# Kernel optimization log

Measured on AMD Instinct MI355X. Metric: run time of the kernel, lower is better.

Reference implementation:

```python
import jax, jax.numpy as jnp
import numpy as np

N = 50000      # nodes
E = 800000     # edges
F = 128        # node_features
DSS = 64       # degree_set_size
H = 128        # latent dim (hardcoded in GraphES)


def gcn_conv(x, W, b, src, dst, n):
    # PyG GCNConv: linear -> symmetric-normalized aggregation with self loops -> bias
    h = x @ W                                            # [N, C_out]
    deg = jnp.zeros((n,), x.dtype).at[dst].add(1.0) + 1.0  # in-degree incl. self loop
    dinv = jax.lax.rsqrt(deg)
    norm = dinv[src] * dinv[dst]                         # [E]
    agg = jnp.zeros_like(h).at[dst].add(h[src] * norm[:, None])
    agg = agg + h * (dinv * dinv)[:, None]               # self-loop term (norm_ii = 1/deg_i)
    return agg + b


def mlp(x, w1, b1, w2, b2):
    return jax.nn.relu(x @ w1 + b1) @ w2 + b2


def _swap(ei, i1, i2, coin):
    e1 = jnp.take(ei, i1, axis=1)
    e2 = jnp.take(ei, i2, axis=1)
    a, b = e1[0], e1[1]
    c, d = e2[0], e2[1]
    ne1 = jnp.where(coin, jnp.stack([a, d]), jnp.stack([a, c]))
    ne2 = jnp.where(coin, jnp.stack([c, b]), jnp.stack([b, d]))
    return ei.at[:, i1].set(ne1).at[:, i2].set(ne2)


def setup_inputs() -> dict:
    key = jax.random.key(0)
    ks = jax.random.split(key, 24)
    s = 0.05

    def rn(k, shape):
        return jax.random.normal(k, shape, jnp.float32) * s

    return {
        "x": jax.random.normal(ks[0], (N, F), jnp.float32),
        "edge_index": jax.random.randint(ks[1], (2, E), 0, N, dtype=jnp.int32),
        "degree_set": jax.random.randint(ks[2], (N,), 0, DSS, dtype=jnp.int32),
        "timesteps": 5,
        # encoder: GCN(F+DSS -> 2H), GCN(2H -> H)
        "enc_w1": rn(ks[3], (F + DSS, 2 * H)), "enc_b1": jnp.zeros((2 * H,), jnp.float32),
        "enc_w2": rn(ks[4], (2 * H, H)),       "enc_b2": jnp.zeros((H,), jnp.float32),
        # decoder: GCN(H+DSS -> 2F), GCN(2F -> F)
        "dec_w1": rn(ks[5], (H + DSS, 2 * F)), "dec_b1": jnp.zeros((2 * F,), jnp.float32),
        "dec_w2": rn(ks[6], (2 * F, F)),       "dec_b2": jnp.zeros((F,), jnp.float32),
        # edge_predictor_1: Linear(128,64)->ReLU->Linear(64,1)
        "ep1_w1": rn(ks[7], (H, 64)),  "ep1_b1": jnp.zeros((64,), jnp.float32),
        "ep1_w2": rn(ks[8], (64, 1)),  "ep1_b2": jnp.zeros((1,), jnp.float32),
        # edge_predictor_2: input is z concat flattened pair features -> 128+256=384
        "ep2_w1": rn(ks[9], (H + 2 * H, 64)), "ep2_b1": jnp.zeros((64,), jnp.float32),
        "ep2_w2": rn(ks[10], (64, 1)),        "ep2_b2": jnp.zeros((1,), jnp.float32),
    }


def reference(x, edge_index, degree_set, timesteps,
              enc_w1, enc_b1, enc_w2, enc_b2,
              dec_w1, dec_b1, dec_w2, dec_b2,
              ep1_w1, ep1_b1, ep1_w2, ep1_b2,
              ep2_w1, ep2_b1, ep2_w2, ep2_b2):
    src, dst = edge_index[0], edge_index[1]
    dh = jax.nn.one_hot(degree_set, DSS, dtype=x.dtype)  # [N, DSS]

    # ---- encoder ----
    h = jax.nn.relu(gcn_conv(jnp.concatenate([x, dh], 1), enc_w1, enc_b1, src, dst, N))
    z = gcn_conv(h, enc_w2, enc_b2, src, dst, N)          # [N, H]

    # ---- forward diffusion: timesteps random edge swaps (deterministic PRNG) ----
    ei = edge_index
    for t in range(timesteps):
        k1, k2 = jax.random.split(jax.random.fold_in(jax.random.key(1), t))
        idx = jax.random.choice(k1, E, (2,), replace=False)
        ei = _swap(ei, idx[0], idx[1], jax.random.bernoulli(k2))

    # ---- reverse process: argmax-driven edge swaps ----
    # edge_predictor_1 scores depend only on z -> identical every step; compute once
    i1 = jnp.argmax(mlp(z, ep1_w1, ep1_b1, ep1_w2, ep1_b2).squeeze(-1))
    for t in range(timesteps):
        e1 = jnp.take(ei, i1, axis=1)                     # [2]
        e1f = z[e1].reshape(-1)                           # [2H]
        cond = jnp.concatenate([z, jnp.broadcast_to(e1f, (N, 2 * H))], 1)
        i2 = jnp.argmax(mlp(cond, ep2_w1, ep2_b1, ep2_w2, ep2_b2).squeeze(-1))
        coin = jax.random.bernoulli(jax.random.fold_in(jax.random.key(2), t))
        ei = _swap(ei, i1, i2, coin)

    # ---- decoder on final edge structure ----
    src2, dst2 = ei[0], ei[1]
    hd = jax.nn.relu(gcn_conv(jnp.concatenate([z, dh], 1), dec_w1, dec_b1, src2, dst2, N))
    out = gcn_conv(hd, dec_w2, dec_b2, src2, dst2, N)     # [N, F]
    return out, ei
```

## Files before the change

kernel.cpp:

```cpp
#include <hip/hip_runtime.h>
#include <cstdint>
#include <cstddef>
#include <vector>
#include <algorithm>

#define NN 50000
#define EE 800000
#define FF 128
#define HH 128
#define TSTEPS 5

typedef __attribute__((ext_vector_type(8))) short bf16x8;
typedef __attribute__((ext_vector_type(4))) float f32x4;

__device__ __forceinline__ float bf2f(unsigned short u)
{
    return __uint_as_float((unsigned)u << 16);
}
__device__ __forceinline__ unsigned short f2bf(float x)
{
    unsigned u = __float_as_uint(x);
    u = (u + 0x7FFFu + ((u >> 16) & 1u));
    return (unsigned short)(u >> 16);
}
__device__ __forceinline__ void splitbf(float v, unsigned short& hi, unsigned short& lo)
{
    hi = f2bf(v);
    lo = f2bf(v - bf2f(hi));
}

__device__ __forceinline__ void gload16(const void* g, void* l)
{
    __builtin_amdgcn_global_load_lds(
        (const __attribute__((address_space(1))) void*)g,
        (__attribute__((address_space(3))) void*)l, 16, 0, 0);
}

__global__ __launch_bounds__(256, 4) void zw1_gemm(
    const float* __restrict__ A, const float* __restrict__ Wp4,
    float* __restrict__ Pout, int n, const float* __restrict__ bias)
{
    __shared__ float As[32][128];
    const int row0 = blockIdx.x * 32;
    const int tid = threadIdx.x;
    for (int idx = tid; idx < 32 * 32; idx += 256) {
        int r = idx >> 5, k4 = idx & 31;
        int gr = row0 + r;
        float4 v = make_float4(0.f, 0.f, 0.f, 0.f);
        if (gr < n) v = ((const float4*)(A + (size_t)gr * 128))[k4];
        *(float4*)&As[r][k4 * 4] = v;
    }
    __syncthreads();
    const int w = tid >> 6, l = tid & 63;
    float acc[8];
#pragma unroll
    for (int r = 0; r < 8; r++) acc[r] = 0.f;

#pragma unroll 2
    for (int k4 = 0; k4 < 32; k4++) {
        float4 wv = ((const float4*)Wp4)[k4 * 64 + l];
#pragma unroll
        for (int r = 0; r < 8; r++) {
            float4 zv = *(const float4*)&As[w * 8 + r][k4 * 4];
            acc[r] = fmaf(zv.x, wv.x, acc[r]);
            acc[r] = fmaf(zv.y, wv.y, acc[r]);
            acc[r] = fmaf(zv.z, wv.z, acc[r]);
            acc[r] = fmaf(zv.w, wv.w, acc[r]);
        }
    }
    float bv = bias[l];
#pragma unroll
    for (int r = 0; r < 8; r++) {
        int gr = row0 + w * 8 + r;
        if (gr < n) Pout[(size_t)gr * 64 + l] = acc[r] + bv;
    }
}

template <int K, int C, int BC, int WR, int WC, bool HAS_BIAS, bool RELU>
__global__ __launch_bounds__(256) void gemm_bf16_tiled(
    const unsigned short* __restrict__ A, const unsigned short* __restrict__ Wp,
    unsigned short* __restrict__ Pout, const float* __restrict__ bias, int n)
{
    constexpr int KC = K / 32;
    constexpr int RT = 128 / (WR * 16);
    constexpr int TT = BC / (WC * 16);
    constexpr int STAGE_USHORTS = 4096 + BC * 32;
    constexpr int OT_USHORTS = 128 * BC;
    constexpr int LDS_USHORTS = (STAGE_USHORTS > OT_USHORTS) ? STAGE_USHORTS : OT_USHORTS;
    __shared__ __align__(16) unsigned short smem[LDS_USHORTS];
    unsigned short* AL = smem;
    unsigned short* WL = smem + 4096;

    const int row0 = blockIdx.x * 128;
    const int col0 = blockIdx.y * BC;
    const int tid = threadIdx.x;
    const int w = tid >> 6, l = tid & 63;
    const int m = l & 15, quad = l >> 4;
    const int wr = w / WC, wc = w % WC;
    const int rowBase = wr * (RT * 16);
    const int colBase = wc * (TT * 16);

    f32x4 acc[RT][TT];
#pragma unroll
    for (int rt = 0; rt < RT; rt++)
#pragma unroll
        for (int tt = 0; tt < TT; tt++) acc[rt][tt] = { 0.f, 0.f, 0.f, 0.f };

    for (int kc = 0; kc < KC; kc++) {
        for (int s = w; s < 8; s += 4) {
            int rg = row0 + s * 16 + (l >> 2);
            if (rg > n - 1) rg = n - 1;
            size_t go = (size_t)rg * K + kc * 32 + (l & 3) * 8;
            gload16(A + go, AL + s * 512);
        }
        for (int s = w; s < BC / 16; s += 4) {
            size_t wo = ((size_t)kc * C + col0) * 32 + s * 512 + l * 8;
            gload16(Wp + wo, WL + s * 512);
        }
        __syncthreads();

        bf16x8 a[RT];
#pragma unroll
        for (int rt = 0; rt < RT; rt++)
            a[rt] = *(const bf16x8*)(AL + (rowBase + rt * 16 + m) * 32 + quad * 8);
#pragma unroll
        for (int tt = 0; tt < TT; tt++) {
            bf16x8 b = *(const bf16x8*)(WL + (colBase + tt * 16 + m) * 32 + quad * 8);
#pragma unroll
            for (int rt = 0; rt < RT; rt++)
                acc[rt][tt] = __builtin_amdgcn_mfma_f32_16x16x32_bf16(a[rt], b, acc[rt][tt], 0, 0, 0);
        }
        __syncthreads();
    }

    unsigned short* Ot = smem;
#pragma unroll
    for (int tt = 0; tt < TT; tt++) {
        int col_in = colBase + tt * 16 + m;
        float bv = HAS_BIAS ? bias[col0 + col_in] : 0.f;
#pragma unroll
        for (int rt = 0; rt < RT; rt++)
#pragma unroll
            for (int r = 0; r < 4; r++) {
                int row_in = rowBase + rt * 16 + quad * 4 + r;
                float v = acc[rt][tt][r] + bv;
                if (RELU) v = fmaxf(v, 0.f);
                Ot[row_in * BC + col_in] = f2bf(v);
            }
    }
    __syncthreads();
    for (int idx = tid; idx < 128 * (BC / 8); idx += 256) {
        int rr = idx / (BC / 8), c8 = idx - rr * (BC / 8);
        int gr = row0 + rr;
        if (gr < n)
            *(bf16x8*)(Pout + (size_t)gr * C + col0 + c8 * 8) =
                *(const bf16x8*)(Ot + rr * BC + c8 * 8);
    }
}

template <int K, int C, int BC, int WR, int WC, bool HAS_BIAS, bool RELU, bool OUT_SPLIT>
__global__ __launch_bounds__(256) void gemm_split_tiled(
    const unsigned short* __restrict__ Ahi, const unsigned short* __restrict__ Alo,
    const unsigned short* __restrict__ Whi, const unsigned short* __restrict__ Wlo,
    void* __restrict__ PoutHi, unsigned short* __restrict__ PoutLo,
    const float* __restrict__ bias, int n)
{
    constexpr int KC = K / 32;
    constexpr int RT = 128 / (WR * 16);
    constexpr int TT = BC / (WC * 16);
    constexpr int LDS_USHORTS = 8192 + BC * 64;
    __shared__ __align__(16) unsigned short smem[LDS_USHORTS];
    unsigned short* AhL = smem;
    unsigned short* AlL = smem + 4096;
    unsigned short* WhL = smem + 8192;
    unsigned short* WlL = smem + 8192 + BC * 32;

    const int row0 = blockIdx.x * 128;
    const int col0 = blockIdx.y * BC;
    const int tid = threadIdx.x;
    const int w = tid >> 6, l = tid & 63;
    const int m = l & 15, quad = l >> 4;
    const int wr = w / WC, wc = w % WC;
    const int rowBase = wr * (RT * 16);
    const int colBase = wc * (TT * 16);

    f32x4 acc[RT][TT];
#pragma unroll
    for (int rt = 0; rt < RT; rt++)
#pragma unroll
        for (int tt = 0; tt < TT; tt++) acc[rt][tt] = { 0.f, 0.f, 0.f, 0.f };

    for (int kc = 0; kc < KC; kc++) {
        for (int s = w; s < 8; s += 4) {
            int rg = row0 + s * 16 + (l >> 2);
            if (rg > n - 1) rg = n - 1;
            size_t go = (size_t)rg * K + kc * 32 + (l & 3) * 8;
            gload16(Ahi + go, AhL + s * 512);
            gload16(Alo + go, AlL + s * 512);
        }
        for (int s = w; s < BC / 16; s += 4) {
            size_t wo = ((size_t)kc * C + col0) * 32 + s * 512 + l * 8;
            gload16(Whi + wo, WhL + s * 512);
            gload16(Wlo + wo, WlL + s * 512);
        }
        __syncthreads();

        bf16x8 ah[RT], al[RT];
#pragma unroll
        for (int rt = 0; rt < RT; rt++) {
            int ro = (rowBase + rt * 16 + m) * 32 + quad * 8;
            ah[rt] = *(const bf16x8*)(AhL + ro);
            al[rt] = *(const bf16x8*)(AlL + ro);
        }
#pragma unroll
        for (int tt = 0; tt < TT; tt++) {
            int co = (colBase + tt * 16 + m) * 32 + quad * 8;
            bf16x8 wh = *(const bf16x8*)(WhL + co);
            bf16x8 wl = *(const bf16x8*)(WlL + co);
#pragma unroll
            for (int rt = 0; rt < RT; rt++) {
                acc[rt][tt] = __builtin_amdgcn_mfma_f32_16x16x32_bf16(al[rt], wh, acc[rt][tt], 0, 0, 0);
                acc[rt][tt] = __builtin_amdgcn_mfma_f32_16x16x32_bf16(ah[rt], wl, acc[rt][tt], 0, 0, 0);
                acc[rt][tt] = __builtin_amdgcn_mfma_f32_16x16x32_bf16(ah[rt], wh, acc[rt][tt], 0, 0, 0);
            }
        }
        __syncthreads();
    }

    if (OUT_SPLIT) {
        unsigned short* Ot = smem;
#pragma unroll
        for (int tt = 0; tt < TT; tt++) {
            int col_in = colBase + tt * 16 + m;
            float bv = HAS_BIAS ? bias[col0 + col_in] : 0.f;
#pragma unroll
            for (int rt = 0; rt < RT; rt++)
#pragma unroll
                for (int r = 0; r < 4; r++) {
                    int row_in = rowBase + rt * 16 + quad * 4 + r;
                    float v = acc[rt][tt][r] + bv;
                    if (RELU) v = fmaxf(v, 0.f);
                    Ot[row_in * BC + col_in] = f2bf(v);
                }
        }
        __syncthreads();
        for (int idx = tid; idx < 128 * (BC / 8); idx += 256) {
            int rr = idx / (BC / 8), c8 = idx - rr * (BC / 8);
            int gr = row0 + rr;
            if (gr < n)
                *(bf16x8*)((unsigned short*)PoutHi + (size_t)gr * C + col0 + c8 * 8) =
                    *(const bf16x8*)(Ot + rr * BC + c8 * 8);
        }
        __syncthreads();
#pragma unroll
        for (int tt = 0; tt < TT; tt++) {
            int col_in = colBase + tt * 16 + m;
            float bv = HAS_BIAS ? bias[col0 + col_in] : 0.f;
#pragma unroll
            for (int rt = 0; rt < RT; rt++)
#pragma unroll
                for (int r = 0; r < 4; r++) {
                    int row_in = rowBase + rt * 16 + quad * 4 + r;
                    float v = acc[rt][tt][r] + bv;
                    if (RELU) v = fmaxf(v, 0.f);
                    unsigned short h = f2bf(v);
                    Ot[row_in * BC + col_in] = f2bf(v - bf2f(h));
                }
        }
        __syncthreads();
        for (int idx = tid; idx < 128 * (BC / 8); idx += 256) {
            int rr = idx / (BC / 8), c8 = idx - rr * (BC / 8);
            int gr = row0 + rr;
            if (gr < n)
                *(bf16x8*)(PoutLo + (size_t)gr * C + col0 + c8 * 8) =
                    *(const bf16x8*)(Ot + rr * BC + c8 * 8);
        }
    } else {
#pragma unroll
        for (int tt = 0; tt < TT; tt++) {
            int col = col0 + colBase + tt * 16 + m;
            float bv = HAS_BIAS ? bias[col] : 0.f;
#pragma unroll
            for (int rt = 0; rt < RT; rt++)
#pragma unroll
                for (int r = 0; r < 4; r++) {
                    int gr = row0 + rowBase + rt * 16 + quad * 4 + r;
                    if (gr >= n) continue;
                    float v = acc[rt][tt][r] + bv;
                    if (RELU) v = fmaxf(v, 0.f);
                    ((float*)PoutHi)[(size_t)gr * C + col] = v;
                }
        }
    }
}

template <int K, int C>
__global__ void pack_w(const float* __restrict__ W, unsigned short* __restrict__ Wp)
{
    int idx = blockIdx.x * 256 + threadIdx.x;
    if (idx >= K * C) return;
    int k = idx / C, nn = idx - k * C;
    Wp[((size_t)(k >> 5) * C + nn) * 32 + (k & 31)] = f2bf(W[idx]);
}

template <int K, int C>
__global__ void pack_w_split(const float* __restrict__ W,
                             unsigned short* __restrict__ Wphi,
                             unsigned short* __restrict__ Wplo)
{
    int idx = blockIdx.x * 256 + threadIdx.x;
    if (idx >= K * C) return;
    int k = idx / C, nn = idx - k * C;
    unsigned short hi, lo;
    splitbf(W[idx], hi, lo);
    size_t o = ((size_t)(k >> 5) * C + nn) * 32 + (k & 31);
    Wphi[o] = hi;
    Wplo[o] = lo;
}

template <int K, int C>
__global__ void pack_w4(const float* __restrict__ W, float* __restrict__ Wp4)
{
    int idx = blockIdx.x * 256 + threadIdx.x;
    if (idx >= K * C) return;
    int k = idx / C, c = idx - k * C;
    Wp4[(((size_t)(k >> 2) * C) + c) * 4 + (k & 3)] = W[idx];
}

__global__ void count_deg(const int* __restrict__ dst, int* __restrict__ cnt, int e)
{
    int i = blockIdx.x * blockDim.x + threadIdx.x;
    if (i < e) {
        unsigned d = (unsigned)dst[i];
        if (d < (unsigned)NN) atomicAdd(&cnt[d], 1);
    }
}

__global__ void scan_block(const int* __restrict__ cnt, int* __restrict__ excl,
                           int* __restrict__ bsum, float* __restrict__ dinv, int n)
{
    __shared__ int s[256];
    int i = blockIdx.x * 256 + threadIdx.x;
    int v = (i < n) ? cnt[i] : 0;
    if (i < n) dinv[i] = 1.0f / sqrtf((float)v + 1.0f);
    s[threadIdx.x] = v;
    __syncthreads();
    for (int off = 1; off < 256; off <<= 1) {
        int t = (threadIdx.x >= off) ? s[threadIdx.x - off] : 0;
        __syncthreads();
        s[threadIdx.x] += t;
        __syncthreads();
    }
    if (i < n) excl[i] = s[threadIdx.x] - v;
    if (threadIdx.x == 255) bsum[blockIdx.x] = s[255];
}
__global__ void scan_add_fill(int* __restrict__ rowptr, const int* __restrict__ bsum,
                              int* __restrict__ fill, int n, int e)
{
    int pre = 0;
    for (int b = 0; b < (int)blockIdx.x; b++) pre += bsum[b];
    int i = blockIdx.x * 256 + threadIdx.x;
    if (i < n) { rowptr[i] += pre; fill[i] = 0; }
    if (i == 0) rowptr[n] = e;
}

__global__ void csr_fill_pairs(const int* __restrict__ src, const int* __restrict__ dst,
                               const float* __restrict__ dinv, const int* __restrict__ rowptr,
                               int* __restrict__ fill, int2* __restrict__ csr_pair, int e)
{
    int i = blockIdx.x * blockDim.x + threadIdx.x;
    if (i >= e) return;
    int d = dst[i], s = src[i];
    if ((unsigned)d >= (unsigned)NN || (unsigned)s >= (unsigned)NN) return;
    int slot = rowptr[d] + atomicAdd(&fill[d], 1);
    csr_pair[slot] = make_int2(s, __float_as_int(dinv[s] * dinv[d]));
}

template <bool BF16SRC, int OUTMODE>
__global__ __launch_bounds__(256) void agg_feat(
    const void* __restrict__ Xv, const int* __restrict__ ds,
    const int* __restrict__ rowptr, const int2* __restrict__ csr_pair,
    const float* __restrict__ dinv,
    void* __restrict__ Fout, unsigned short* __restrict__ FoutLo)
{
    const int w = threadIdx.x >> 6, l = threadIdx.x & 63;
    const int i = blockIdx.x * 4 + w;
    if (i >= NN) return;
    const int half = l >> 5, lh = l & 31;

    auto loadRow4 = [&](int s, float* v) {
        if (BF16SRC) {
            ushort4 u = ((const ushort4*)((const unsigned short*)Xv + (size_t)s * 128))[lh];
            v[0] = bf2f(u.x); v[1] = bf2f(u.y); v[2] = bf2f(u.z); v[3] = bf2f(u.w);
        } else {
            float4 t = ((const float4*)((const float*)Xv + (size_t)s * 128))[lh];
            v[0] = t.x; v[1] = t.y; v[2] = t.z; v[3] = t.w;
        }
    };

    float di = dinv[i], d2 = di * di;
    float acc[4];
    {
        float sv[4];
        loadRow4(i, sv);
        float wgt = half ? 0.f : d2;
#pragma unroll
        for (int v = 0; v < 4; v++) acc[v] = sv[v] * wgt;
    }
    float hist = (ds[i] == l) ? d2 : 0.f;

    const int beg = rowptr[i], end = rowptr[i + 1];
    int idx = beg;
    for (; idx + 8 <= end; idx += 8) {
        int s[8]; float nw[8]; int b[8];
#pragma unroll
        for (int j = 0; j < 8; j++) {
            int2 pr = csr_pair[idx + j];
            s[j] = pr.x; nw[j] = __int_as_float(pr.y);
        }
#pragma unroll
        for (int j = 0; j < 8; j++) b[j] = ds[s[j]];
        float vv[4][4];
#pragma unroll
        for (int p = 0; p < 4; p++) loadRow4(s[2 * p + half], vv[p]);
#pragma unroll
        for (int p = 0; p < 4; p++) {
            float wp = nw[2 * p + half];
#pragma unroll
            for (int v = 0; v < 4; v++) acc[v] = fmaf(vv[p][v], wp, acc[v]);
        }
#pragma unroll
        for (int j = 0; j < 8; j++) hist += (b[j] == l) ? nw[j] : 0.f;
    }
    for (; idx + 2 <= end; idx += 2) {
        int2 p0 = csr_pair[idx], p1 = csr_pair[idx + 1];
        int s0 = p0.x, s1 = p1.x;
        float n0 = __int_as_float(p0.y), n1 = __int_as_float(p1.y);
        int b0 = ds[s0], b1 = ds[s1];
        float v0[4];
        loadRow4(half ? s1 : s0, v0);
        float wp = half ? n1 : n0;
#pragma unroll
        for (int v = 0; v < 4; v++) acc[v] = fmaf(v0[v], wp, acc[v]);
        hist += (b0 == l) ? n0 : 0.f;
        hist += (b1 == l) ? n1 : 0.f;
    }
    if (idx < end) {
        int2 p0 = csr_pair[idx];
        int s0 = p0.x;
        float n0 = __int_as_float(p0.y);
        int b0 = ds[s0];
        float v0[4];
        loadRow4(s0, v0);
        float wp = half ? 0.f : n0;
#pragma unroll
        for (int v = 0; v < 4; v++) acc[v] = fmaf(v0[v], wp, acc[v]);
        hist += (b0 == l) ? n0 : 0.f;
    }
#pragma unroll
    for (int v = 0; v < 4; v++) acc[v] += __shfl_xor(acc[v], 32, 64);

    if (OUTMODE == 2) {
        if (half == 0) {
            unsigned short h[4], lo[4];
#pragma unroll
            for (int v = 0; v < 4; v++) splitbf(acc[v], h[v], lo[v]);
            ((ushort4*)((unsigned short*)Fout + (size_t)i * 192))[lh] =
                make_ushort4(h[0], h[1], h[2], h[3]);
            ((ushort4*)(FoutLo + (size_t)i * 192))[lh] =
                make_ushort4(lo[0], lo[1], lo[2], lo[3]);
        }
        unsigned short hh, ll;
        splitbf(hist, hh, ll);
        ((unsigned short*)Fout)[(size_t)i * 192 + 128 + l] = hh;
        FoutLo[(size_t)i * 192 + 128 + l] = ll;
    } else if (OUTMODE == 1) {
        if (half == 0) {
            ((ushort4*)((unsigned short*)Fout + (size_t)i * 192))[lh] =
                make_ushort4(f2bf(acc[0]), f2bf(acc[1]), f2bf(acc[2]), f2bf(acc[3]));
        }
        ((unsigned short*)Fout)[(size_t)i * 192 + 128 + l] = f2bf(hist);
    } else {
        if (half == 0) {
            ((float4*)((float*)Fout + (size_t)i * 192))[lh] =
                make_float4(acc[0], acc[1], acc[2], acc[3]);
        }
        ((float*)Fout)[(size_t)i * 192 + 128 + l] = hist;
    }
}

template <bool RELU, bool BF16P, bool CLAMP>
__global__ __launch_bounds__(256) void agg_wave(
    const void* __restrict__ Pv, const int* __restrict__ rowptr,
    const int2* __restrict__ csr_pair,
    const float* __restrict__ dinv, const float* __restrict__ bias,
    float* __restrict__ B, unsigned short* __restrict__ Bbf)
{
    const int w = threadIdx.x >> 6, l = threadIdx.x & 63;
    const int i = blockIdx.x * 4 + w;
    if (i >= NN) return;
    const int half = l >> 5, lh = l & 31;

    auto loadRow4 = [&](int s, float* v) {
        if (BF16P) {
            ushort4 u = ((const ushort4*)((const unsigned short*)Pv + (size_t)s * 128))[lh];
            v[0] = bf2f(u.x); v[1] = bf2f(u.y); v[2] = bf2f(u.z); v[3] = bf2f(u.w);
        } else {
            float4 t = ((const float4*)((const float*)Pv + (size_t)s * 128))[lh];
            v[0] = t.x; v[1] = t.y; v[2] = t.z; v[3] = t.w;
        }
    };

    float di = dinv[i], d2 = di * di;
    float acc[4];
    {
        float sv[4];
        loadRow4(i, sv);
        float wgt = half ? 0.f : d2;
#pragma unroll
        for (int v = 0; v < 4; v++) acc[v] = sv[v] * wgt;
    }

    const int beg = rowptr[i], end = rowptr[i + 1];
    int idx = beg;
    for (; idx + 8 <= end; idx += 8) {
        int s[8]; float nw[8];
#pragma unroll
        for (int j = 0; j < 8; j++) {
            int2 pr = csr_pair[idx + j];
            s[j] = pr.x; nw[j] = __int_as_float(pr.y);
        }
        float vv[4][4];
#pragma unroll
        for (int p = 0; p < 4; p++) loadRow4(s[2 * p + half], vv[p]);
#pragma unroll
        for (int p = 0; p < 4; p++) {
            float wp = nw[2 * p + half];
#pragma unroll
            for (int v = 0; v < 4; v++) acc[v] = fmaf(vv[p][v], wp, acc[v]);
        }
    }
    for (; idx + 2 <= end; idx += 2) {
        int2 p0 = csr_pair[idx], p1 = csr_pair[idx + 1];
        int s0 = p0.x, s1 = p1.x;
        float n0 = __int_as_float(p0.y), n1 = __int_as_float(p1.y);
        float v0[4];
        loadRow4(half ? s1 : s0, v0);
        float wp = half ? n1 : n0;
#pragma unroll
        for (int v = 0; v < 4; v++) acc[v] = fmaf(v0[v], wp, acc[v]);
    }
    if (idx < end) {
        int2 p0 = csr_pair[idx];
        int s0 = p0.x;
        float n0 = __int_as_float(p0.y);
        float v0[4];
        loadRow4(s0, v0);
        float wp = half ? 0.f : n0;
#pragma unroll
        for (int v = 0; v < 4; v++) acc[v] = fmaf(v0[v], wp, acc[v]);
    }
#pragma unroll
    for (int v = 0; v < 4; v++) acc[v] += __shfl_xor(acc[v], 32, 64);

    if (half == 0) {
        float r[4];
#pragma unroll
        for (int v = 0; v < 4; v++) {
            r[v] = acc[v] + bias[lh * 4 + v];
            if (RELU) r[v] = fmaxf(r[v], 0.f);
            if (CLAMP) r[v] = fminf(fmaxf(r[v], -64.f), 64.f);
        }
        ((float4*)(B + (size_t)i * 128))[lh] = make_float4(r[0], r[1], r[2], r[3]);
        if (Bbf)
            ((ushort4*)(Bbf + (size_t)i * 128))[lh] =
                make_ushort4(f2bf(r[0]), f2bf(r[1]), f2bf(r[2]), f2bf(r[3]));
    }
}

__device__ __forceinline__ unsigned long long packScore(float s, int i)
{
    unsigned u = __float_as_uint(s);
    u = (u & 0x80000000u) ? ~u : (u | 0x80000000u);
    return ((unsigned long long)u << 32) | (unsigned)(~(unsigned)i);
}
__device__ __forceinline__ int unpackIdx(unsigned long long v)
{
    return (int)(~(unsigned)(v & 0xFFFFFFFFull));
}
__device__ __forceinline__ unsigned long long maxu64(unsigned long long a,
                                                     unsigned long long b)
{
    return a > b ? a : b;
}

__device__ __forceinline__ void publishBest(
    unsigned long long* blockBest, unsigned* counter, unsigned long long bv,
    int nblocks, unsigned* isLastFlag)
{
    __hip_atomic_store(&blockBest[blockIdx.x], bv, __ATOMIC_RELEASE,
                       __HIP_MEMORY_SCOPE_AGENT);
    unsigned prev = __hip_atomic_fetch_add(counter, 1u, __ATOMIC_ACQ_REL,
                                           __HIP_MEMORY_SCOPE_AGENT);
    *isLastFlag = (prev == (unsigned)(nblocks - 1)) ? 1u : 0u;
}
__device__ __forceinline__ unsigned long long loadBest(
    const unsigned long long* blockBest, int i)
{
    return __hip_atomic_load(&blockBest[i], __ATOMIC_RELAXED,
                             __HIP_MEMORY_SCOPE_AGENT);
}

__global__ __launch_bounds__(256, 4) void score1_blocks(
    const float* __restrict__ z, const float* __restrict__ w1p4,
    const float* __restrict__ b1, const float* __restrict__ w2,
    unsigned long long* __restrict__ blockBest,
    unsigned long long* __restrict__ out, unsigned* __restrict__ counter,
    int n, int nblocks)
{
    __shared__ float Zs[64][HH];
    __shared__ unsigned long long red[4];
    __shared__ unsigned isLast;
    const int row0 = blockIdx.x * 64;
    const int tid = threadIdx.x;
    for (int idx = tid; idx < 64 * 32; idx += 256) {
        int r = idx >> 5, k4 = idx & 31;
        int gr = row0 + r;
        float4 v = make_float4(0.f, 0.f, 0.f, 0.f);
        if (gr < n) v = ((const float4*)(z + (size_t)gr * HH))[k4];
        *(float4*)&Zs[r][k4 * 4] = v;
    }
    __syncthreads();

    const int w = tid >> 6, l = tid & 63;
    float b1v = b1[l], w2v = w2[l];
    unsigned long long best = 0;
    for (int rg = 0; rg < 4; rg++) {
        const int rbase = w * 16 + rg * 4;
        float acc[4];
#pragma unroll
        for (int r = 0; r < 4; r++) acc[r] = b1v;
#pragma unroll 4
        for (int k4 = 0; k4 < 32; k4++) {
            float4 wv = ((const float4*)w1p4)[k4 * 64 + l];
#pragma unroll
            for (int r = 0; r < 4; r++) {
                float4 zv = *(const float4*)&Zs[rbase + r][k4 * 4];
                acc[r] = fmaf(zv.x, wv.x, acc[r]);
                acc[r] = fmaf(zv.y, wv.y, acc[r]);
                acc[r] = fmaf(zv.z, wv.z, acc[r]);
                acc[r] = fmaf(zv.w, wv.w, acc[r]);
            }
        }
#pragma unroll
        for (int r = 0; r < 4; r++) {
            float p = fmaxf(acc[r], 0.f) * w2v;
#pragma unroll
            for (int off = 32; off > 0; off >>= 1) p += __shfl_xor(p, off, 64);
            int row = row0 + rbase + r;
            if (row < n) best = maxu64(best, packScore(p, row));
        }
    }
    if (l == 0) red[w] = best;
    __syncthreads();
    if (tid == 0) {
        unsigned long long bv = maxu64(maxu64(red[0], red[1]), maxu64(red[2], red[3]));
        publishBest(blockBest, counter, bv, nblocks, &isLast);
    }
    __syncthreads();
    if (isLast) {
        unsigned long long b = 0;
        for (int i = tid; i < nblocks; i += 256) b = maxu64(b, loadBest(blockBest, i));
#pragma unroll
        for (int off = 32; off > 0; off >>= 1)
            b = maxu64(b, (unsigned long long)__shfl_xor((long long)b, off, 64));
        if ((tid & 63) == 0) red[tid >> 6] = b;
        __syncthreads();
        if (tid == 0) {
            *out = maxu64(maxu64(red[0], red[1]), maxu64(red[2], red[3]));
            __hip_atomic_store(counter, 0u, __ATOMIC_RELAXED, __HIP_MEMORY_SCOPE_AGENT);
        }
    }
}

__global__ __launch_bounds__(256) void score2_fused(
    int* __restrict__ ei, const unsigned long long* __restrict__ best1,
    const float* __restrict__ z, const float* __restrict__ w1,
    const float* __restrict__ zw1, const float* __restrict__ w2,
    unsigned long long* __restrict__ blockBest, unsigned* __restrict__ counter,
    int n, int coin)
{
    __shared__ float za_s[HH], zb_s[HH];
    __shared__ float cpart[4][64];
    __shared__ float Cs[64], W2s[64];
    __shared__ unsigned long long red[4];
    __shared__ unsigned isLast;
    int i1 = unpackIdx(*best1);
    if ((unsigned)i1 >= (unsigned)EE) i1 = 0;
    int a = ei[i1], b = ei[EE + i1];
    if ((unsigned)a >= (unsigned)NN) a = 0;
    if ((unsigned)b >= (unsigned)NN) b = 0;
    const int tid = threadIdx.x;
    if (tid < HH) za_s[tid] = z[(size_t)a * HH + tid];
    else          zb_s[tid - HH] = z[(size_t)b * HH + tid - HH];
    __syncthreads();
    const int h = tid & 63, kg = tid >> 6;
    float accc = 0.f;
#pragma unroll
    for (int kk = 0; kk < 32; kk++) {
        int k = kg * 32 + kk;
        accc = fmaf(za_s[k], w1[(128 + k) * 64 + h], accc);
        accc = fmaf(zb_s[k], w1[(256 + k) * 64 + h], accc);
    }
    cpart[kg][h] = accc;
    __syncthreads();
    if (tid < 64) {
        Cs[tid] = (cpart[0][tid] + cpart[1][tid]) + (cpart[2][tid] + cpart[3][tid]);
        W2s[tid] = w2[tid];
    }
    __syncthreads();
    const int w = kg, l = h;
    unsigned long long best = 0;
    for (int i = blockIdx.x * 4 + w; i < n; i += gridDim.x * 4) {
        float v = zw1[(size_t)i * 64 + l] + Cs[l];
        v = fmaxf(v, 0.f) * W2s[l];
#pragma unroll
        for (int off = 32; off > 0; off >>= 1) v += __shfl_xor(v, off, 64);
        best = maxu64(best, packScore(v, i));
    }
    if (l == 0) red[w] = best;
    __syncthreads();
    const int nblocks = (int)gridDim.x;
    if (tid == 0) {
        unsigned long long bv = maxu64(maxu64(red[0], red[1]), maxu64(red[2], red[3]));
        publishBest(blockBest, counter, bv, nblocks, &isLast);
    }
    __syncthreads();
    if (isLast) {
        unsigned long long bb = 0;
        for (int i = tid; i < nblocks; i += 256) bb = maxu64(bb, loadBest(blockBest, i));
#pragma unroll
        for (int off = 32; off > 0; off >>= 1)
            bb = maxu64(bb, (unsigned long long)__shfl_xor((long long)bb, off, 64));
        if ((tid & 63) == 0) red[tid >> 6] = bb;
        __syncthreads();
        if (tid == 0) {
            unsigned long long bestv = maxu64(maxu64(red[0], red[1]), maxu64(red[2], red[3]));
            int i2 = unpackIdx(bestv);
            if ((unsigned)i2 >= (unsigned)EE) i2 = 0;
            int A = ei[i1], B = ei[EE + i1], C = ei[i2], D = ei[EE + i2];
            ei[i1] = A;             ei[EE + i1] = coin ? D : C;
            ei[i2] = coin ? C : B;  ei[EE + i2] = coin ? B : D;
            __hip_atomic_store(counter, 0u, __ATOMIC_RELAXED, __HIP_MEMORY_SCOPE_AGENT);
        }
    }
}

struct Swaps { int a[TSTEPS]; int b[TSTEPS]; unsigned coins; };

__global__ void fwd_swaps_k(int* __restrict__ ei, Swaps s)
{
    if (threadIdx.x != 0 || blockIdx.x != 0) return;
    for (int t = 0; t < TSTEPS; t++) {
        int i1 = s.a[t], i2 = s.b[t];
        if ((unsigned)i1 >= (unsigned)EE || (unsigned)i2 >= (unsigned)EE) continue;
        int coin = (s.coins >> t) & 1;
        int A = ei[i1], B = ei[EE + i1], C = ei[i2], D = ei[EE + i2];
        ei[i1] = A;             ei[EE + i1] = coin ? D : C;
        ei[i2] = coin ? C : B;  ei[EE + i2] = coin ? B : D;
    }
}

__global__ void write_edges(const int* __restrict__ ei, float* __restrict__ dst)
{
    int i = blockIdx.x * 256 + threadIdx.x;
    if (i < 2 * EE) dst[i] = (float)ei[i];
}

static inline uint32_t rotl32(uint32_t x, int n) { return (x << n) | (x >> (32 - n)); }

static void tf(uint32_t k0, uint32_t k1, uint32_t c0, uint32_t c1,
               uint32_t& o0, uint32_t& o1)
{
    uint32_t ks[3] = { k0, k1, k0 ^ k1 ^ 0x1BD11BDAu };
    uint32_t x0 = c0 + ks[0], x1 = c1 + ks[1];
    static const int rA[4] = { 13, 15, 26, 6 };
    static const int rB[4] = { 17, 29, 16, 24 };
    for (int g = 0; g < 5; g++) {
        const int* r = (g & 1) ? rB : rA;
        for (int j = 0; j < 4; j++) { x0 += x1; x1 = rotl32(x1, r[j]); x1 ^= x0; }
        x0 += ks[(g + 1) % 3];
        x1 += ks[(g + 2) % 3] + (uint32_t)(g + 1);
    }
    o0 = x0; o1 = x1;
}

static void jsplit_part(uint32_t k0, uint32_t k1,
                        uint32_t& a0, uint32_t& a1, uint32_t& b0, uint32_t& b1)
{
    tf(k0, k1, 0u, 0u, a0, a1);
    tf(k0, k1, 0u, 1u, b0, b1);
}

static void jbits_part(uint32_t k0, uint32_t k1, uint32_t n, std::vector<uint32_t>& out)
{
    out.resize(n);
    for (uint32_t i = 0; i < n; i++) {
        uint32_t a, b;
        tf(k0, k1, 0u, i, a, b);
        out[i] = a ^ b;
    }
}

static bool jbern_part(uint32_t k0, uint32_t k1)
{
    uint32_t a, b;
    tf(k0, k1, 0u, 0u, a, b);
    return (a ^ b) < 0x80000000u;
}

struct PrngConsts {
    Swaps swaps;
    int revCoin[TSTEPS];
    PrngConsts()
    {
        swaps.coins = 0;
        std::vector<uint32_t> bits1, bits2;
        std::vector<uint64_t> packed((size_t)EE);
        for (int t = 0; t < TSTEPS; t++) {
            uint32_t kt0, kt1;
            tf(0u, 1u, 0u, (uint32_t)t, kt0, kt1);
            uint32_t kc0, kc1, kb0, kb1;
            jsplit_part(kt0, kt1, kc0, kc1, kb0, kb1);
            if (jbern_part(kb0, kb1)) swaps.coins |= (1u << t);

            uint32_t cur0 = kc0, cur1 = kc1, sub0, sub1, nk0, nk1;
            jsplit_part(cur0, cur1, nk0, nk1, sub0, sub1);
            cur0 = nk0; cur1 = nk1;
            jbits_part(sub0, sub1, EE, bits1);
            jsplit_part(cur0, cur1, nk0, nk1, sub0, sub1);
            cur0 = nk0; cur1 = nk1;
            jbits_part(sub0, sub1, EE, bits2);

            uint64_t m1 = ~0ull, m2 = ~0ull;
            for (uint32_t pos = 0; pos < EE; pos++) {
                uint64_t u = ((uint64_t)bits2[pos] << 32) | pos;
                if (u < m1) { m2 = m1; m1 = u; }
                else if (u < m2) { m2 = u; }
            }
            uint32_t pos0 = (uint32_t)m1, pos1 = (uint32_t)m2;
            for (uint32_t j = 0; j < EE; j++)
                packed[j] = ((uint64_t)bits1[j] << 32) | j;
            std::nth_element(packed.begin(), packed.begin() + pos0, packed.end());
            uint32_t j0 = (uint32_t)packed[pos0];
            std::nth_element(packed.begin(), packed.begin() + pos1, packed.end());
            uint32_t j1 = (uint32_t)packed[pos1];
            swaps.a[t] = (int)j0;
            swaps.b[t] = (int)j1;
        }
        for (int t = 0; t < TSTEPS; t++) {
            uint32_t kt0, kt1;
            tf(0u, 2u, 0u, (uint32_t)t, kt0, kt1);
            revCoin[t] = jbern_part(kt0, kt1) ? 1 : 0;
        }
    }
};
static const PrngConsts g_prng;

extern "C" void kernel_launch(void* const* d_in, const int* in_sizes, int n_in,
                              void* d_out, int out_size, void* d_ws, size_t ws_size,
                              hipStream_t stream)
{
    (void)out_size; (void)ws_size;

    static const int kWant[20] = {
        NN * FF, 2 * EE, NN, 1,
        192 * 256, 256, 256 * 128, 128,
        192 * 256, 256, 256 * 128, 128,
        128 * 64, 64, 64, 1,
        384 * 64, 64, 64, 1
    };
    const void* p[20] = {};
    {
        int j = 0;
        for (int k = 0; k < 20; k++) {
            if (j < n_in && in_sizes[j] == kWant[k]) { p[k] = d_in[j]; j++; }
            else if (kWant[k] == 1)                  { p[k] = nullptr; }
            else if (j < n_in)                       { p[k] = d_in[j]; j++; }
        }
    }
    const float* x      = (const float*)p[0];
    const int*   ei_in  = (const int*)p[1];
    const int*   ds     = (const int*)p[2];
    const float* enc_w1 = (const float*)p[4];
    const float* enc_b1 = (const float*)p[5];
    const float* enc_w2 = (const float*)p[6];
    const float* enc_b2 = (const float*)p[7];
    const float* dec_w1 = (const float*)p[8];
    const float* dec_b1 = (const float*)p[9];
    const float* dec_w2 = (const float*)p[10];
    const float* dec_b2 = (const float*)p[11];
    const float* ep1_w1 = (const float*)p[12];
    const float* ep1_b1 = (const float*)p[13];
    const float* ep1_w2 = (const float*)p[14];
    const float* ep2_w1 = (const float*)p[16];
    const float* ep2_b1 = (const float*)p[17];
    const float* ep2_w2 = (const float*)p[18];

    char* ws = (char*)d_ws;
    size_t off = 0;
    auto alloc = [&](size_t bytes) -> void* {
        void* q = ws + off;
        off += (bytes + 255) & ~(size_t)255;
        return q;
    };
    float* bufP    = (float*)alloc((size_t)NN * 256 * 4);
    float* bufH    = (float*)alloc((size_t)NN * 256 * 4);
    int*   eiw     = (int*)alloc((size_t)2 * EE * 4);
    int2*  csr_pair = (int2*)alloc((size_t)EE * 8);
    int*   rowptr  = (int*)alloc((size_t)(NN + 1) * 4);
    int*   cnt     = (int*)alloc((size_t)NN * 4);
    int*   fill    = (int*)alloc((size_t)NN * 4);
    int*   bsum    = (int*)alloc(256 * 4);
    float* dinv    = (float*)alloc((size_t)NN * 4);
    unsigned short* zbf   = (unsigned short*)alloc((size_t)NN * 128 * 2);
    unsigned short* wp1   = (unsigned short*)alloc((size_t)192 * 256 * 2);
    unsigned short* wp2   = (unsigned short*)alloc((size_t)256 * 128 * 2);
    unsigned short* w1hi  = (unsigned short*)alloc((size_t)192 * 256 * 2);
    unsigned short* w1lo  = (unsigned short*)alloc((size_t)192 * 256 * 2);
    unsigned short* w2hi  = (unsigned short*)alloc((size_t)256 * 128 * 2);
    unsigned short* w2lo  = (unsigned short*)alloc((size_t)256 * 128 * 2);
    float* ep1w1p = (float*)alloc((size_t)128 * 64 * 4);
    float* ep2w1p = (float*)alloc((size_t)128 * 64 * 4);
    unsigned long long* blockBest = (unsigned long long*)alloc(4096 * 8);
    unsigned long long* best1 = (unsigned long long*)alloc(8);
    unsigned* counters = (unsigned*)alloc(256);

    unsigned short* f1hi = (unsigned short*)bufP;
    unsigned short* f1lo = f1hi + (size_t)NN * 192;
    float* P2   = bufP;
    float* zw1  = bufP;
    unsigned short* feat2bf = (unsigned short*)bufP;
    unsigned short* p4      = (unsigned short*)bufP;
    unsigned short* hhi = (unsigned short*)bufH;
    unsigned short* hlo = hhi + (size_t)NN * 256;
    float* zbuf = bufH;
    unsigned short* hdbf = (unsigned short*)bufH;

    const int TPB = 256;
    const int gN      = (NN + TPB - 1) / TPB;
    const int gE      = (EE + TPB - 1) / TPB;
    const int gRows64s = (NN + 63) / 64;
    const int gRows32 = (NN + 31) / 32;
    const int gRows128 = (NN + 127) / 128;
    const int gWave   = (NN + 3) / 4;

    hipMemsetAsync(counters, 0, 8, stream);

    pack_w<192, 256><<<(192 * 256 + TPB - 1) / TPB, TPB, 0, stream>>>(dec_w1, wp1);
    pack_w<256, 128><<<(256 * 128 + TPB - 1) / TPB, TPB, 0, stream>>>(dec_w2, wp2);
    pack_w_split<192, 256><<<(192 * 256 + TPB - 1) / TPB, TPB, 0, stream>>>(enc_w1, w1hi, w1lo);
    pack_w_split<256, 128><<<(256 * 128 + TPB - 1) / TPB, TPB, 0, stream>>>(enc_w2, w2hi, w2lo);
    pack_w4<128, 64><<<(128 * 64 + TPB - 1) / TPB, TPB, 0, stream>>>(ep1_w1, ep1w1p);
    pack_w4<128, 64><<<(128 * 64 + TPB - 1) / TPB, TPB, 0, stream>>>(ep2_w1, ep2w1p);

    hipMemsetAsync(cnt, 0, (size_t)NN * 4, stream);
    count_deg<<<gE, TPB, 0, stream>>>(ei_in + EE, cnt, EE);
    scan_block<<<gN, TPB, 0, stream>>>(cnt, rowptr, bsum, dinv, NN);
    scan_add_fill<<<gN, TPB, 0, stream>>>(rowptr, bsum, fill, NN, EE);
    csr_fill_pairs<<<gE, TPB, 0, stream>>>(ei_in, ei_in + EE, dinv, rowptr, fill,
                                           csr_pair, EE);

    agg_feat<false, 2><<<gWave, TPB, 0, stream>>>(
        x, ds, rowptr, csr_pair, dinv, f1hi, f1lo);
    gemm_split_tiled<192, 256, 128, 2, 2, true, true, true>
        <<<dim3(gRows128, 2), TPB, 0, stream>>>(
        f1hi, f1lo, w1hi, w1lo, hhi, hlo, enc_b1, NN);

    gemm_split_tiled<256, 128, 64, 4, 1, false, false, false>
        <<<dim3(gRows128, 2), TPB, 0, stream>>>(
        hhi, hlo, w2hi, w2lo, P2, nullptr, nullptr, NN);
    agg_wave<false, false, false><<<gWave, TPB, 0, stream>>>(
        P2, rowptr, csr_pair, dinv, enc_b2, zbuf, zbf);

    score1_blocks<<<gRows64s, TPB, 0, stream>>>(zbuf, ep1w1p, ep1_b1, ep1_w2,
                                                blockBest, best1, counters + 0,
                                                NN, gRows64s);
    zw1_gemm<<<gRows32, TPB, 0, stream>>>(zbuf, ep2w1p, zw1, NN, ep2_b1);

    hipMemcpyAsync(eiw, ei_in, (size_t)2 * EE * 4, hipMemcpyDeviceToDevice, stream);
    fwd_swaps_k<<<1, 64, 0, stream>>>(eiw, g_prng.swaps);

    for (int t = 0; t < TSTEPS; t++) {
        score2_fused<<<256, TPB, 0, stream>>>(eiw, best1, zbuf, ep2_w1,
                                              zw1, ep2_w2, blockBest, counters + 1,
                                              NN, g_prng.revCoin[t]);
    }

    hipMemsetAsync(cnt, 0, (size_t)NN * 4, stream);
    count_deg<<<gE, TPB, 0, stream>>>(eiw + EE, cnt, EE);
    scan_block<<<gN, TPB, 0, stream>>>(cnt, rowptr, bsum, dinv, NN);
    scan_add_fill<<<gN, TPB, 0, stream>>>(rowptr, bsum, fill, NN, EE);
    csr_fill_pairs<<<gE, TPB, 0, stream>>>(eiw, eiw + EE, dinv, rowptr, fill,
                                           csr_pair, EE);

    agg_feat<true, 1><<<gWave, TPB, 0, stream>>>(
        zbf, ds, rowptr, csr_pair, dinv, feat2bf, nullptr);
    gemm_bf16_tiled<192, 256, 128, 2, 2, true, true>
        <<<dim3(gRows128, 2), TPB, 0, stream>>>(
        feat2bf, wp1, hdbf, dec_b1, NN);

    gemm_bf16_tiled<256, 128, 128, 2, 2, false, false>
        <<<dim3(gRows128, 1), TPB, 0, stream>>>(
        hdbf, wp2, p4, nullptr, NN);
    agg_wave<false, true, true><<<gWave, TPB, 0, stream>>>(
        p4, rowptr, csr_pair, dinv, dec_b2, (float*)d_out, nullptr);

    write_edges<<<(2 * EE + TPB - 1) / TPB, TPB, 0, stream>>>(
        eiw, (float*)d_out + (size_t)NN * FF);
}
```

Baseline: 797.1 us.

## Patch degree counts incrementally across swaps and pack degree bucket into CSR

Instead of recounting in-degrees from scratch after the edge swaps, the initial degree counts are copied and patched in the single-thread swap kernels, which removes a memset and a full-edge atomic count_deg pass. Separately, each node's degree-set bucket is packed into the high bits of the CSR source index, so the aggregation kernel no longer does a dependent gather from ds per edge. The packing relies on node ids fitting in 20 bits and ds values being small and non-negative.

```diff
diff --git a/kernel.cpp b/kernel.cpp
--- a/kernel.cpp
+++ b/kernel.cpp
@@ -337,12 +337,16 @@
 }
 
 __global__ void scan_block(const int* __restrict__ cnt, int* __restrict__ excl,
-                           int* __restrict__ bsum, float* __restrict__ dinv, int n)
+                           int* __restrict__ bsum, float* __restrict__ dinv,
+                           int* __restrict__ cnt_copy, int n)
 {
     __shared__ int s[256];
     int i = blockIdx.x * 256 + threadIdx.x;
     int v = (i < n) ? cnt[i] : 0;
-    if (i < n) dinv[i] = 1.0f / sqrtf((float)v + 1.0f);
+    if (i < n) {
+        dinv[i] = 1.0f / sqrtf((float)v + 1.0f);
+        if (cnt_copy) cnt_copy[i] = v;
+    }
     s[threadIdx.x] = v;
     __syncthreads();
     for (int off = 1; off < 256; off <<= 1) {
@@ -365,6 +369,7 @@
 }
 
 __global__ void csr_fill_pairs(const int* __restrict__ src, const int* __restrict__ dst,
+                               const int* __restrict__ ds,
                                const float* __restrict__ dinv, const int* __restrict__ rowptr,
                                int* __restrict__ fill, int2* __restrict__ csr_pair, int e)
 {
@@ -373,7 +378,7 @@
     int d = dst[i], s = src[i];
     if ((unsigned)d >= (unsigned)NN || (unsigned)s >= (unsigned)NN) return;
     int slot = rowptr[d] + atomicAdd(&fill[d], 1);
-    csr_pair[slot] = make_int2(s, __float_as_int(dinv[s] * dinv[d]));
+    csr_pair[slot] = make_int2(s | (ds[s] << 20), __float_as_int(dinv[s] * dinv[d]));
 }
 
 template <bool BF16SRC, int OUTMODE>
@@ -416,10 +421,9 @@
 #pragma unroll
         for (int j = 0; j < 8; j++) {
             int2 pr = csr_pair[idx + j];
-            s[j] = pr.x; nw[j] = __int_as_float(pr.y);
-        }
-#pragma unroll
-        for (int j = 0; j < 8; j++) b[j] = ds[s[j]];
+            s[j] = pr.x & 0xFFFFF; b[j] = pr.x >> 20;
+            nw[j] = __int_as_float(pr.y);
+        }
         float vv[4][4];
 #pragma unroll
         for (int p = 0; p < 4; p++) loadRow4(s[2 * p + half], vv[p]);
@@ -434,9 +438,9 @@
     }
     for (; idx + 2 <= end; idx += 2) {
         int2 p0 = csr_pair[idx], p1 = csr_pair[idx + 1];
-        int s0 = p0.x, s1 = p1.x;
+        int s0 = p0.x & 0xFFFFF, s1 = p1.x & 0xFFFFF;
+        int b0 = p0.x >> 20, b1 = p1.x >> 20;
         float n0 = __int_as_float(p0.y), n1 = __int_as_float(p1.y);
-        int b0 = ds[s0], b1 = ds[s1];
         float v0[4];
         loadRow4(half ? s1 : s0, v0);
         float wp = half ? n1 : n0;
@@ -447,9 +451,9 @@
     }
     if (idx < end) {
         int2 p0 = csr_pair[idx];
-        int s0 = p0.x;
+        int s0 = p0.x & 0xFFFFF;
+        int b0 = p0.x >> 20;
         float n0 = __int_as_float(p0.y);
-        int b0 = ds[s0];
         float v0[4];
         loadRow4(s0, v0);
         float wp = half ? 0.f : n0;
@@ -528,7 +532,7 @@
 #pragma unroll
         for (int j = 0; j < 8; j++) {
             int2 pr = csr_pair[idx + j];
-            s[j] = pr.x; nw[j] = __int_as_float(pr.y);
+            s[j] = pr.x & 0xFFFFF; nw[j] = __int_as_float(pr.y);
         }
         float vv[4][4];
 #pragma unroll
@@ -542,7 +546,7 @@
     }
     for (; idx + 2 <= end; idx += 2) {
         int2 p0 = csr_pair[idx], p1 = csr_pair[idx + 1];
-        int s0 = p0.x, s1 = p1.x;
+        int s0 = p0.x & 0xFFFFF, s1 = p1.x & 0xFFFFF;
         float n0 = __int_as_float(p0.y), n1 = __int_as_float(p1.y);
         float v0[4];
         loadRow4(half ? s1 : s0, v0);
@@ -552,7 +556,7 @@
     }
     if (idx < end) {
         int2 p0 = csr_pair[idx];
-        int s0 = p0.x;
+        int s0 = p0.x & 0xFFFFF;
         float n0 = __int_as_float(p0.y);
         float v0[4];
         loadRow4(s0, v0);
@@ -609,6 +613,16 @@
 {
     return __hip_atomic_load(&blockBest[i], __ATOMIC_RELAXED,
                              __HIP_MEMORY_SCOPE_AGENT);
+}
+
+__device__ __forceinline__ void patchDeg(int* cnt2, int i1, int i2,
+                                         int B, int C, int D, int coin)
+{
+    if (i1 == i2) return;
+    int n1 = coin ? D : C;
+    int n2 = coin ? B : D;
+    cnt2[B]--; cnt2[n1]++;
+    cnt2[D]--; cnt2[n2]++;
 }
 
 __global__ __launch_bounds__(256, 4) void score1_blocks(
@@ -688,7 +702,7 @@
     const float* __restrict__ z, const float* __restrict__ w1,
     const float* __restrict__ zw1, const float* __restrict__ w2,
     unsigned long long* __restrict__ blockBest, unsigned* __restrict__ counter,
-    int n, int coin)
+    int* __restrict__ cnt2, int n, int coin)
 {
     __shared__ float za_s[HH], zb_s[HH];
     __shared__ float cpart[4][64];
@@ -751,6 +765,7 @@
             int A = ei[i1], B = ei[EE + i1], C = ei[i2], D = ei[EE + i2];
             ei[i1] = A;             ei[EE + i1] = coin ? D : C;
             ei[i2] = coin ? C : B;  ei[EE + i2] = coin ? B : D;
+            patchDeg(cnt2, i1, i2, B, C, D, coin);
             __hip_atomic_store(counter, 0u, __ATOMIC_RELAXED, __HIP_MEMORY_SCOPE_AGENT);
         }
     }
@@ -758,7 +773,7 @@
 
 struct Swaps { int a[TSTEPS]; int b[TSTEPS]; unsigned coins; };
 
-__global__ void fwd_swaps_k(int* __restrict__ ei, Swaps s)
+__global__ void fwd_swaps_k(int* __restrict__ ei, int* __restrict__ cnt2, Swaps s)
 {
     if (threadIdx.x != 0 || blockIdx.x != 0) return;
     for (int t = 0; t < TSTEPS; t++) {
@@ -768,6 +783,7 @@
         int A = ei[i1], B = ei[EE + i1], C = ei[i2], D = ei[EE + i2];
         ei[i1] = A;             ei[EE + i1] = coin ? D : C;
         ei[i2] = coin ? C : B;  ei[EE + i2] = coin ? B : D;
+        patchDeg(cnt2, i1, i2, B, C, D, coin);
     }
 }
 
@@ -920,6 +936,7 @@
     int2*  csr_pair = (int2*)alloc((size_t)EE * 8);
     int*   rowptr  = (int*)alloc((size_t)(NN + 1) * 4);
     int*   cnt     = (int*)alloc((size_t)NN * 4);
+    int*   cnt2    = (int*)alloc((size_t)NN * 4);
     int*   fill    = (int*)alloc((size_t)NN * 4);
     int*   bsum    = (int*)alloc(256 * 4);
     float* dinv    = (float*)alloc((size_t)NN * 4);
@@ -966,9 +983,9 @@
 
     hipMemsetAsync(cnt, 0, (size_t)NN * 4, stream);
     count_deg<<<gE, TPB, 0, stream>>>(ei_in + EE, cnt, EE);
-    scan_block<<<gN, TPB, 0, stream>>>(cnt, rowptr, bsum, dinv, NN);
+    scan_block<<<gN, TPB, 0, stream>>>(cnt, rowptr, bsum, dinv, cnt2, NN);
     scan_add_fill<<<gN, TPB, 0, stream>>>(rowptr, bsum, fill, NN, EE);
-    csr_fill_pairs<<<gE, TPB, 0, stream>>>(ei_in, ei_in + EE, dinv, rowptr, fill,
+    csr_fill_pairs<<<gE, TPB, 0, stream>>>(ei_in, ei_in + EE, ds, dinv, rowptr, fill,
                                            csr_pair, EE);
 
     agg_feat<false, 2><<<gWave, TPB, 0, stream>>>(
@@ -989,19 +1006,17 @@
     zw1_gemm<<<gRows32, TPB, 0, stream>>>(zbuf, ep2w1p, zw1, NN, ep2_b1);
 
     hipMemcpyAsync(eiw, ei_in, (size_t)2 * EE * 4, hipMemcpyDeviceToDevice, stream);
-    fwd_swaps_k<<<1, 64, 0, stream>>>(eiw, g_prng.swaps);
+    fwd_swaps_k<<<1, 64, 0, stream>>>(eiw, cnt2, g_prng.swaps);
 
     for (int t = 0; t < TSTEPS; t++) {
         score2_fused<<<256, TPB, 0, stream>>>(eiw, best1, zbuf, ep2_w1,
                                               zw1, ep2_w2, blockBest, counters + 1,
-                                              NN, g_prng.revCoin[t]);
-    }
-
-    hipMemsetAsync(cnt, 0, (size_t)NN * 4, stream);
-    count_deg<<<gE, TPB, 0, stream>>>(eiw + EE, cnt, EE);
-    scan_block<<<gN, TPB, 0, stream>>>(cnt, rowptr, bsum, dinv, NN);
+                                              cnt2, NN, g_prng.revCoin[t]);
+    }
+
+    scan_block<<<gN, TPB, 0, stream>>>(cnt2, rowptr, bsum, dinv, nullptr, NN);
     scan_add_fill<<<gN, TPB, 0, stream>>>(rowptr, bsum, fill, NN, EE);
-    csr_fill_pairs<<<gE, TPB, 0, stream>>>(eiw, eiw + EE, dinv, rowptr, fill,
+    csr_fill_pairs<<<gE, TPB, 0, stream>>>(eiw, eiw + EE, ds, dinv, rowptr, fill,
                                            csr_pair, EE);
 
     agg_feat<true, 1><<<gWave, TPB, 0, stream>>>(
```

After: 766.8 us. 1.04x faster.
